# Kernel optimization log

Hardware: AMD Instinct MI355X
Metric: run time of the kernel (lower is better)

Reference implementation:

```python
import jax, jax.numpy as jnp
import numpy as np

SIZE_IN = 4096
SIZE_OUT = 4096
BATCH = 4096


def setup_inputs() -> dict:
    key = jax.random.key(0)
    k1, k2, k3, k4, k5, k6 = jax.random.split(key, 6)
    mu_in = jax.random.normal(k1, (BATCH, SIZE_IN), dtype=jnp.float32)
    sigma_in = jax.random.uniform(k2, (BATCH, SIZE_IN), dtype=jnp.float32)
    # parameters, initialized as in the torch module
    w_mu = 5e-05 * jax.random.normal(k3, (SIZE_IN, SIZE_OUT), dtype=jnp.float32)
    w_sigma = jax.random.uniform(k4, (SIZE_IN * SIZE_OUT,), dtype=jnp.float32,
                                 minval=-12.0, maxval=-2.2)
    b_mu = 5e-05 * jax.random.normal(k5, (SIZE_OUT,), dtype=jnp.float32)
    b_sigma = jax.random.uniform(k6, (SIZE_OUT,), dtype=jnp.float32,
                                 minval=-12.0, maxval=-10.0)
    return {"mu_in": mu_in, "sigma_in": sigma_in, "w_mu": w_mu,
            "w_sigma": w_sigma, "b_mu": b_mu, "b_sigma": b_sigma}


def reference(mu_in, sigma_in, w_mu, w_sigma, b_mu, b_sigma):
    # mean path: mu_out[b,o] = sum_i mu_in[b,i] * w_mu[i,o] + b_mu[o]
    mu_out = jnp.einsum('bi,io->bo', mu_in, w_mu) + b_mu
    # variance path: x diag(softplus(w_sigma)) x^T, per output feature.
    # Equivalent to (mu_in^2) @ softplus(w_sigma).reshape(size_in, size_out),
    # avoiding the quadratic diag_embed + bmm materialization.
    sigma_w = jax.nn.softplus(w_sigma).reshape(SIZE_IN, SIZE_OUT)
    Sigma_out = jnp.einsum('bi,io->bo', mu_in * mu_in, sigma_w) + jax.nn.softplus(b_sigma)
    # KL loss, verbatim from the torch code
    sp = jax.nn.softplus(w_sigma)
    term1 = SIZE_IN * jnp.log(sp)
    term2 = jnp.sum(jnp.abs(w_mu))
    term3 = SIZE_IN * sp
    kl_loss = -0.5 * jnp.mean(term1 - term2 - term3)
    return (mu_out, Sigma_out, kl_loss)
```

## Files before the change

kernel.cpp:

```cpp
#include <hip/hip_runtime.h>
#include <hip/hip_bf16.h>
#include <math.h>

#define M_BATCH   4096
#define K_IN      4096
#define N_OUT     4096
#define NELEM     16777216

typedef __bf16 bf16;
typedef bf16  bf16x8 __attribute__((ext_vector_type(8)));
typedef float f32x4  __attribute__((ext_vector_type(4)));

__device__ __forceinline__ float softplus_fast(float x) {
    if (x > 15.f) return x;
    const float e = __expf(x);
    if (e < 0.0883f)
        return e * (1.f + e * (-0.5f + e * 0.3333333f));
    return __logf(1.f + e);
}

__device__ __forceinline__ unsigned short f2bf_bits(float x) {
    bf16 b = (bf16)x;
    return __builtin_bit_cast(unsigned short, b);
}

__device__ __forceinline__ void gload_lds16(const void* g, void* l) {
    __builtin_amdgcn_global_load_lds(
        (__attribute__((address_space(1))) void*)g,
        (__attribute__((address_space(3))) void*)l,
        16, 0, 0);
}

__global__ __launch_bounds__(256) void prep_a(const float4* __restrict__ mu,
                                              ushort4* __restrict__ A,
                                              ushort4* __restrict__ A2) {
    const int i = blockIdx.x * 256 + threadIdx.x;
    const float4 v = mu[i];
    ushort4 a, a2;
    a.x  = f2bf_bits(v.x);       a.y  = f2bf_bits(v.y);
    a.z  = f2bf_bits(v.z);       a.w  = f2bf_bits(v.w);
    a2.x = f2bf_bits(v.x * v.x); a2.y = f2bf_bits(v.y * v.y);
    a2.z = f2bf_bits(v.z * v.z); a2.w = f2bf_bits(v.w * v.w);
    A[i]  = a;
    A2[i] = a2;
}

__global__ __launch_bounds__(256) void prep_w(const float* __restrict__ wmu,
                                              const float* __restrict__ wsg,
                                              bf16* __restrict__ Wmu_t,
                                              bf16* __restrict__ Wsg_t,
                                              float* __restrict__ partials) {
    __shared__ bf16 tmu[64][65];
    __shared__ bf16 tsg[64][65];
    __shared__ float red[256];

    const int t  = threadIdx.x;
    const int ti = blockIdx.y;
    const int tj = blockIdx.x;
    const int r  = t >> 4;
    const int c4 = (t & 15) << 2;

    float s_abs = 0.f, s_sp = 0.f, s_log = 0.f;

    for (int rr = 0; rr < 64; rr += 16) {
        const int row = rr + r;
        const size_t goff = (size_t)(ti * 64 + row) * N_OUT + tj * 64 + c4;
        const float4 vm = *(const float4*)(wmu + goff);
        const float4 vs = *(const float4*)(wsg + goff);
        const float sp0 = softplus_fast(vs.x), sp1 = softplus_fast(vs.y);
        const float sp2 = softplus_fast(vs.z), sp3 = softplus_fast(vs.w);
        s_abs += fabsf(vm.x) + fabsf(vm.y) + fabsf(vm.z) + fabsf(vm.w);
        s_sp  += sp0 + sp1 + sp2 + sp3;
        s_log += __logf(sp0) + __logf(sp1) + __logf(sp2) + __logf(sp3);
        tmu[row][c4 + 0] = (bf16)vm.x; tmu[row][c4 + 1] = (bf16)vm.y;
        tmu[row][c4 + 2] = (bf16)vm.z; tmu[row][c4 + 3] = (bf16)vm.w;
        tsg[row][c4 + 0] = (bf16)sp0;  tsg[row][c4 + 1] = (bf16)sp1;
        tsg[row][c4 + 2] = (bf16)sp2;  tsg[row][c4 + 3] = (bf16)sp3;
    }
    __syncthreads();

    for (int cc = 0; cc < 64; cc += 16) {
        const int j  = cc + r;
        const int i0 = c4;
        ushort4 om, os;
        om.x = __builtin_bit_cast(unsigned short, tmu[i0 + 0][j]);
        om.y = __builtin_bit_cast(unsigned short, tmu[i0 + 1][j]);
        om.z = __builtin_bit_cast(unsigned short, tmu[i0 + 2][j]);
        om.w = __builtin_bit_cast(unsigned short, tmu[i0 + 3][j]);
        os.x = __builtin_bit_cast(unsigned short, tsg[i0 + 0][j]);
        os.y = __builtin_bit_cast(unsigned short, tsg[i0 + 1][j]);
        os.z = __builtin_bit_cast(unsigned short, tsg[i0 + 2][j]);
        os.w = __builtin_bit_cast(unsigned short, tsg[i0 + 3][j]);
        const size_t o = (size_t)(tj * 64 + j) * K_IN + ti * 64 + i0;
        *(ushort4*)(Wmu_t + o) = om;
        *(ushort4*)(Wsg_t + o) = os;
    }

    const int bid = blockIdx.y * 64 + blockIdx.x;
    float vals[3] = { s_log, s_sp, s_abs };
    for (int v = 0; v < 3; v++) {
        __syncthreads();
        red[t] = vals[v];
        __syncthreads();
        for (int s = 128; s > 0; s >>= 1) {
            if (t < s) red[t] += red[t + s];
            __syncthreads();
        }
        if (t == 0) partials[v * 4096 + bid] = red[0];
    }
}

__global__ __launch_bounds__(256) void gemm_bf16(const bf16* __restrict__ A1,
                                                 const bf16* __restrict__ Bt1,
                                                 const float* __restrict__ bias1,
                                                 float* __restrict__ C1,
                                                 const bf16* __restrict__ A2_,
                                                 const bf16* __restrict__ Bt2,
                                                 const float* __restrict__ bias2,
                                                 float* __restrict__ C2) {
    __shared__ bf16 As[128 * 32];
    __shared__ bf16 Bs[128 * 32];

    const int z = blockIdx.z;
    const bf16*  A    = z ? A2_   : A1;
    const bf16*  Bt   = z ? Bt2   : Bt1;
    const float* bias = z ? bias2 : bias1;
    float*       C    = z ? C2    : C1;

    const int t = threadIdx.x;
    const int rowBase = blockIdx.y * 128;
    const int colBase = blockIdx.x * 128;

    const int srow  = t >> 2;
    const int cg    = ((t & 3) - ((t >> 3) & 3)) & 3;
    const char* agp = (const char*)(A  + (size_t)(rowBase + srow) * K_IN) + (cg << 4);
    const char* bgp = (const char*)(Bt + (size_t)(colBase + srow) * K_IN) + (cg << 4);
    char* alp = (char*)As + t * 16;
    char* blp = (char*)Bs + t * 16;
    const size_t rowskip = (size_t)64 * K_IN * 2;

    const int lane = t & 63;
    const int wave = t >> 6;
    const int wm = (wave >> 1) << 6;
    const int wn = (wave & 1) << 6;
    const int frow = lane & 15;
    const int ko2 = ((((lane >> 4) + (frow >> 1)) & 3) << 3);

    f32x4 zero = { 0.f, 0.f, 0.f, 0.f };
    f32x4 acc[4][4];
#pragma unroll
    for (int i = 0; i < 4; i++)
#pragma unroll
        for (int j = 0; j < 4; j++) acc[i][j] = zero;

    for (int k0 = 0; k0 < K_IN; k0 += 32) {
        const int kb = k0 * 2;
        gload_lds16(agp + kb,            alp);
        gload_lds16(agp + kb + rowskip,  alp + 64 * 64);
        gload_lds16(bgp + kb,            blp);
        gload_lds16(bgp + kb + rowskip,  blp + 64 * 64);
        __syncthreads();

        bf16x8 af[4], bfr[4];
#pragma unroll
        for (int i = 0; i < 4; i++)
            af[i] = *(const bf16x8*)(As + (wm + i * 16 + frow) * 32 + ko2);
#pragma unroll
        for (int j = 0; j < 4; j++)
            bfr[j] = *(const bf16x8*)(Bs + (wn + j * 16 + frow) * 32 + ko2);
#pragma unroll
        for (int i = 0; i < 4; i++)
#pragma unroll
            for (int j = 0; j < 4; j++)
                acc[i][j] = __builtin_amdgcn_mfma_f32_16x16x32_bf16(
                    af[i], bfr[j], acc[i][j], 0, 0, 0);
        __syncthreads();
    }

    const int r0 = (lane >> 4) << 2;
#pragma unroll
    for (int j = 0; j < 4; j++) {
        const int c = colBase + wn + j * 16 + (lane & 15);
        float b = bias[c];
        if (z) b = softplus_fast(b);
#pragma unroll
        for (int i = 0; i < 4; i++) {
            const int rbase = rowBase + wm + i * 16 + r0;
#pragma unroll
            for (int reg = 0; reg < 4; reg++)
                C[(size_t)(rbase + reg) * N_OUT + c] = acc[i][j][reg] + b;
        }
    }
}

__global__ __launch_bounds__(256) void kl_finish(const float* __restrict__ partials,
                                                 const int n,
                                                 float* __restrict__ out) {
    __shared__ double red[256];
    const int t = threadIdx.x;
    double sums[3];
    for (int v = 0; v < 3; v++) {
        double a = 0.0;
        for (int i = t; i < n; i += 256) a += (double)partials[v * n + i];
        red[t] = a;
        __syncthreads();
        for (int s = 128; s > 0; s >>= 1) {
            if (t < s) red[t] += red[t + s];
            __syncthreads();
        }
        sums[v] = red[0];
        __syncthreads();
    }
    if (t == 0) {
        const double mean_log = sums[0] / 16777216.0;
        const double mean_sp  = sums[1] / 16777216.0;
        const double kl = -0.5 * (4096.0 * mean_log - sums[2] - 4096.0 * mean_sp);
        out[0] = (float)kl;
    }
}

__global__ void fb_partials(const float* __restrict__ wmu,
                            const float* __restrict__ wsg,
                            float* __restrict__ partials) {
    __shared__ float red[256];
    const int t = threadIdx.x;
    float s_abs = 0.f, s_sp = 0.f, s_log = 0.f;
    for (int i = blockIdx.x * 256 + t; i < NELEM; i += 1024 * 256) {
        s_abs += fabsf(wmu[i]);
        const float sp = softplus_fast(wsg[i]);
        s_sp += sp;
        s_log += __logf(sp);
    }
    float vals[3] = { s_log, s_sp, s_abs };
    for (int v = 0; v < 3; v++) {
        __syncthreads();
        red[t] = vals[v];
        __syncthreads();
        for (int s = 128; s > 0; s >>= 1) {
            if (t < s) red[t] += red[t + s];
            __syncthreads();
        }
        if (t == 0) partials[v * 1024 + blockIdx.x] = red[0];
    }
}

__global__ void fb_gemm(const float* __restrict__ A,
                        const float* __restrict__ Wm,
                        const float* __restrict__ Ws,
                        const float* __restrict__ bmu,
                        const float* __restrict__ bsg,
                        float* __restrict__ Cmu,
                        float* __restrict__ Csg) {
    __shared__ float As_[16][17], Bm[16][17], Bs_[16][17];
    const int tx = threadIdx.x, ty = threadIdx.y;
    const int row = blockIdx.y * 16 + ty;
    const int col = blockIdx.x * 16 + tx;
    float am = 0.f, as = 0.f;
    for (int k0 = 0; k0 < K_IN; k0 += 16) {
        As_[ty][tx] = A[(size_t)row * K_IN + k0 + tx];
        Bm[ty][tx]  = Wm[(size_t)(k0 + ty) * N_OUT + col];
        Bs_[ty][tx] = softplus_fast(Ws[(size_t)(k0 + ty) * N_OUT + col]);
        __syncthreads();
#pragma unroll
        for (int kk = 0; kk < 16; kk++) {
            const float av = As_[ty][kk];
            am += av * Bm[kk][tx];
            as += av * av * Bs_[kk][tx];
        }
        __syncthreads();
    }
    Cmu[(size_t)row * N_OUT + col] = am + bmu[col];
    Csg[(size_t)row * N_OUT + col] = as + softplus_fast(bsg[col]);
}

extern "C" void kernel_launch(void* const* d_in, const int* in_sizes, int n_in,
                              void* d_out, int out_size, void* d_ws, size_t ws_size,
                              hipStream_t stream) {
    const float* mu_in   = (const float*)d_in[0];
    const float* w_mu    = (const float*)d_in[2];
    const float* w_sigma = (const float*)d_in[3];
    const float* b_mu    = (const float*)d_in[4];
    const float* b_sigma = (const float*)d_in[5];

    float* out_mu  = (float*)d_out;
    float* out_sig = out_mu + (size_t)NELEM;
    float* out_kl  = out_mu + 2 * (size_t)NELEM;

    const size_t mat  = (size_t)NELEM;
    const size_t need = mat * 2 * 4  + 3 * 4096 * sizeof(float);

    if (ws_size >= need) {
        bf16* A      = (bf16*)d_ws;
        bf16* A2     = A + mat;
        bf16* Wmu_t  = A2 + mat;
        bf16* Wsg_t  = Wmu_t + mat;
        float* parts = (float*)(Wsg_t + mat);

        prep_a<<<NELEM / 4 / 256, 256, 0, stream>>>(
            (const float4*)mu_in, (ushort4*)A, (ushort4*)A2);
        prep_w<<<dim3(64, 64), 256, 0, stream>>>(
            w_mu, w_sigma, Wmu_t, Wsg_t, parts);
        gemm_bf16<<<dim3(32, 32, 2), 256, 0, stream>>>(
            A, Wmu_t, b_mu, out_mu, A2, Wsg_t, b_sigma, out_sig);
        kl_finish<<<1, 256, 0, stream>>>(parts, 4096, out_kl);
    } else {
        float* parts = (float*)d_ws;
        fb_partials<<<1024, 256, 0, stream>>>(w_mu, w_sigma, parts);
        fb_gemm<<<dim3(256, 256), dim3(16, 16), 0, stream>>>(
            mu_in, w_mu, w_sigma, b_mu, b_sigma, out_mu, out_sig);
        kl_finish<<<1, 256, 0, stream>>>(parts, 1024, out_kl);
    }
}
```

Measured before the change: 637.5 us.

## Rewrite bf16 GEMM as 256x256 tiles with double-buffered LDS pipeline

The GEMM moves from 128x128 tiles with K=32 steps and 256 threads to 256x256 tiles with K=64 steps and 512 threads (8 waves, each computing 128x64). LDS is double-buffered, and the global-to-LDS loads for the next K tile are interleaved with the MFMA phases. Ordering relies on explicit vmcnt waits, s_barrier, sched_barrier and setprio. The block index is swizzled so neighbouring blocks share L2, and LDS chunks are XOR-swizzled to avoid bank conflicts. Intended gains are more data reuse and hiding memory latency behind compute, at the cost of much higher register and LDS pressure (128 KB of LDS per block) and fragile hand-tuned synchronization.

New measurement: 587.0 us. 7.9% less time.

```diff
diff --git a/kernel.cpp b/kernel.cpp
--- a/kernel.cpp
+++ b/kernel.cpp
@@ -110,16 +110,16 @@
     }
 }
 
-__global__ __launch_bounds__(256) void gemm_bf16(const bf16* __restrict__ A1,
-                                                 const bf16* __restrict__ Bt1,
-                                                 const float* __restrict__ bias1,
-                                                 float* __restrict__ C1,
-                                                 const bf16* __restrict__ A2_,
-                                                 const bf16* __restrict__ Bt2,
-                                                 const float* __restrict__ bias2,
-                                                 float* __restrict__ C2) {
-    __shared__ bf16 As[128 * 32];
-    __shared__ bf16 Bs[128 * 32];
+#define MFMA_BF16 __builtin_amdgcn_mfma_f32_16x16x32_bf16
+
+__global__ __launch_bounds__(512, 2) void gemm_bf16(
+    const bf16* __restrict__ A1,  const bf16* __restrict__ Bt1,
+    const float* __restrict__ bias1, float* __restrict__ C1,
+    const bf16* __restrict__ A2_, const bf16* __restrict__ Bt2,
+    const float* __restrict__ bias2, float* __restrict__ C2) {
+
+    __shared__ bf16 As[2 * 256 * 64];
+    __shared__ bf16 Bs[2 * 256 * 64];
 
     const int z = blockIdx.z;
     const bf16*  A    = z ? A2_   : A1;
@@ -128,69 +128,137 @@
     float*       C    = z ? C2    : C1;
 
     const int t = threadIdx.x;
-    const int rowBase = blockIdx.y * 128;
-    const int colBase = blockIdx.x * 128;
-
-    const int srow  = t >> 2;
-    const int cg    = ((t & 3) - ((t >> 3) & 3)) & 3;
-    const char* agp = (const char*)(A  + (size_t)(rowBase + srow) * K_IN) + (cg << 4);
-    const char* bgp = (const char*)(Bt + (size_t)(colBase + srow) * K_IN) + (cg << 4);
-    char* alp = (char*)As + t * 16;
-    char* blp = (char*)Bs + t * 16;
-    const size_t rowskip = (size_t)64 * K_IN * 2;
+    const int id  = blockIdx.y * 16 + blockIdx.x;
+    const int swz = (id & 7) * 32 + (id >> 3);
+    const int rowBase = (swz >> 4) << 8;
+    const int colBase = (swz & 15) << 8;
+
+    const int srow   = t >> 3;
+    const int schunk = (t & 7) ^ (srow & 7);
+    const char* aG = (const char*)(A  + (size_t)(rowBase + srow) * K_IN + schunk * 8);
+    const char* bG = (const char*)(Bt + (size_t)(colBase + srow) * K_IN + schunk * 8);
+    char* aL = (char*)As + t * 16;
+    char* bL = (char*)Bs + t * 16;
+
+#define STAGE_A(kt, h, par) do {                                               \
+        const size_t kb_ = (size_t)((kt) & 63) << 7;                           \
+        gload_lds16(aG + kb_ + (size_t)(h) * (128 * K_IN * 2),                 \
+                    aL + ((par) << 15) + ((h) << 14));                         \
+        gload_lds16(aG + kb_ + (size_t)(h) * (128 * K_IN * 2) + 64 * K_IN * 2, \
+                    aL + ((par) << 15) + ((h) << 14) + 8192);                  \
+    } while (0)
+#define STAGE_B(kt, h, par) do {                                               \
+        const size_t kb_ = (size_t)((kt) & 63) << 7;                           \
+        gload_lds16(bG + kb_ + (size_t)(h) * (128 * K_IN * 2),                 \
+                    bL + ((par) << 15) + ((h) << 14));                         \
+        gload_lds16(bG + kb_ + (size_t)(h) * (128 * K_IN * 2) + 64 * K_IN * 2, \
+                    bL + ((par) << 15) + ((h) << 14) + 8192);                  \
+    } while (0)
 
     const int lane = t & 63;
     const int wave = t >> 6;
-    const int wm = (wave >> 1) << 6;
-    const int wn = (wave & 1) << 6;
+    const int wr = wave >> 2;
+    const int wc = wave & 3;
     const int frow = lane & 15;
-    const int ko2 = ((((lane >> 4) + (frow >> 1)) & 3) << 3);
-
-    f32x4 zero = { 0.f, 0.f, 0.f, 0.f };
-    f32x4 acc[4][4];
-#pragma unroll
-    for (int i = 0; i < 4; i++)
-#pragma unroll
-        for (int j = 0; j < 4; j++) acc[i][j] = zero;
-
-    for (int k0 = 0; k0 < K_IN; k0 += 32) {
-        const int kb = k0 * 2;
-        gload_lds16(agp + kb,            alp);
-        gload_lds16(agp + kb + rowskip,  alp + 64 * 64);
-        gload_lds16(bgp + kb,            blp);
-        gload_lds16(bgp + kb + rowskip,  blp + 64 * 64);
-        __syncthreads();
-
-        bf16x8 af[4], bfr[4];
-#pragma unroll
-        for (int i = 0; i < 4; i++)
-            af[i] = *(const bf16x8*)(As + (wm + i * 16 + frow) * 32 + ko2);
-#pragma unroll
-        for (int j = 0; j < 4; j++)
-            bfr[j] = *(const bf16x8*)(Bs + (wn + j * 16 + frow) * 32 + ko2);
-#pragma unroll
-        for (int i = 0; i < 4; i++)
-#pragma unroll
-            for (int j = 0; j < 4; j++)
-                acc[i][j] = __builtin_amdgcn_mfma_f32_16x16x32_bf16(
-                    af[i], bfr[j], acc[i][j], 0, 0, 0);
-        __syncthreads();
-    }
+    const int blk0 = (lane >> 4) ^ (lane & 7);
+    const int c0 = blk0 << 4;
+    const int c1 = (blk0 ^ 4) << 4;
+    const char* aRd = (const char*)As + ((wr << 7) + frow) * 128;
+    const char* bRd = (const char*)Bs + ((wc << 6) + frow) * 128;
+
+#define DS_A(par, fi, ck) (*(const bf16x8*)(aRd + ((par) << 15) + ((fi) << 11) + (ck)))
+#define DS_B(par, n,  ck) (*(const bf16x8*)(bRd + ((par) << 15) + ((n)  << 11) + (ck)))
+
+    const f32x4 zero = { 0.f, 0.f, 0.f, 0.f };
+    f32x4 acc[8][4];
+#pragma unroll
+    for (int m = 0; m < 8; ++m)
+#pragma unroll
+        for (int n = 0; n < 4; ++n) acc[m][n] = zero;
+
+#define PHASE(par, q, STAGE_STMT, VM) do {                                        \
+        if ((q) == 0) {                                                           \
+            _Pragma("unroll")                                                     \
+            for (int n = 0; n < 4; ++n) {                                         \
+                bfrag[n][0] = DS_B(par, n, c0);                                   \
+                bfrag[n][1] = DS_B(par, n, c1);                                   \
+            }                                                                     \
+        }                                                                         \
+        const bf16x8 a0k0 = DS_A(par, (q) * 2 + 0, c0);                           \
+        const bf16x8 a0k1 = DS_A(par, (q) * 2 + 0, c1);                           \
+        const bf16x8 a1k0 = DS_A(par, (q) * 2 + 1, c0);                           \
+        const bf16x8 a1k1 = DS_A(par, (q) * 2 + 1, c1);                           \
+        STAGE_STMT;                                                               \
+        if (VM) asm volatile("s_waitcnt vmcnt(4)" ::: "memory");                  \
+        __builtin_amdgcn_sched_barrier(0);                                        \
+        __builtin_amdgcn_s_barrier();                                             \
+        __builtin_amdgcn_sched_barrier(0);                                        \
+        __builtin_amdgcn_s_setprio(1);                                            \
+        _Pragma("unroll")                                                         \
+        for (int n = 0; n < 4; ++n) {                                             \
+            acc[(q)*2+0][n] = MFMA_BF16(a0k0, bfrag[n][0], acc[(q)*2+0][n],0,0,0);\
+            acc[(q)*2+0][n] = MFMA_BF16(a0k1, bfrag[n][1], acc[(q)*2+0][n],0,0,0);\
+            acc[(q)*2+1][n] = MFMA_BF16(a1k0, bfrag[n][0], acc[(q)*2+1][n],0,0,0);\
+            acc[(q)*2+1][n] = MFMA_BF16(a1k1, bfrag[n][1], acc[(q)*2+1][n],0,0,0);\
+        }                                                                         \
+        __builtin_amdgcn_s_setprio(0);                                            \
+        __builtin_amdgcn_sched_barrier(0);                                        \
+        __builtin_amdgcn_s_barrier();                                             \
+        __builtin_amdgcn_sched_barrier(0);                                        \
+    } while (0)
+
+    STAGE_A(0, 0, 0); STAGE_A(0, 1, 0);
+    STAGE_B(0, 0, 0); STAGE_B(0, 1, 0);
+    STAGE_A(1, 0, 1); STAGE_A(1, 1, 1);
+    STAGE_B(1, 0, 1); STAGE_B(1, 1, 1);
+    asm volatile("s_waitcnt vmcnt(8)" ::: "memory");
+    __builtin_amdgcn_sched_barrier(0);
+    __builtin_amdgcn_s_barrier();
+    __builtin_amdgcn_sched_barrier(0);
+
+    for (int i = 0; i < 32; ++i) {
+        const int kA1 = 2 * i + 1;
+        const int kB0 = 2 * i + 2;
+        const int kA0 = 2 * i + 2;
+        const int kB1 = 2 * i + 3;
+        {
+            bf16x8 bfrag[4][2];
+            PHASE(0, 0, STAGE_A(kA1, 0, 1), 0);
+            PHASE(0, 1, STAGE_A(kA1, 1, 1), 0);
+            PHASE(0, 2, STAGE_B(kB0, 0, 0), 0);
+            PHASE(0, 3, STAGE_B(kB0, 1, 0), 1);
+        }
+        {
+            bf16x8 bfrag[4][2];
+            PHASE(1, 0, STAGE_A(kA0, 0, 0), 0);
+            PHASE(1, 1, STAGE_A(kA0, 1, 0), 0);
+            PHASE(1, 2, STAGE_B(kB1, 0, 1), 0);
+            PHASE(1, 3, STAGE_B(kB1, 1, 1), 1);
+        }
+    }
+
+    asm volatile("s_waitcnt vmcnt(0)" ::: "memory");
 
     const int r0 = (lane >> 4) << 2;
-#pragma unroll
-    for (int j = 0; j < 4; j++) {
-        const int c = colBase + wn + j * 16 + (lane & 15);
+    const int ccol = colBase + (wc << 6) + (lane & 15);
+#pragma unroll
+    for (int n = 0; n < 4; ++n) {
+        const int c = ccol + n * 16;
         float b = bias[c];
         if (z) b = softplus_fast(b);
 #pragma unroll
-        for (int i = 0; i < 4; i++) {
-            const int rbase = rowBase + wm + i * 16 + r0;
-#pragma unroll
-            for (int reg = 0; reg < 4; reg++)
-                C[(size_t)(rbase + reg) * N_OUT + c] = acc[i][j][reg] + b;
-        }
-    }
+        for (int m = 0; m < 8; ++m) {
+            const int rbase = rowBase + (wr << 7) + (m << 4) + r0;
+#pragma unroll
+            for (int reg = 0; reg < 4; ++reg)
+                C[(size_t)(rbase + reg) * N_OUT + c] = acc[m][n][reg] + b;
+        }
+    }
+#undef STAGE_A
+#undef STAGE_B
+#undef DS_A
+#undef DS_B
+#undef PHASE
 }
 
 __global__ __launch_bounds__(256) void kl_finish(const float* __restrict__ partials,
@@ -300,7 +368,7 @@
             (const float4*)mu_in, (ushort4*)A, (ushort4*)A2);
         prep_w<<<dim3(64, 64), 256, 0, stream>>>(
             w_mu, w_sigma, Wmu_t, Wsg_t, parts);
-        gemm_bf16<<<dim3(32, 32, 2), 256, 0, stream>>>(
+        gemm_bf16<<<dim3(16, 16, 2), 512, 0, stream>>>(
             A, Wmu_t, b_mu, out_mu, A2, Wsg_t, b_sigma, out_sig);
         kl_finish<<<1, 256, 0, stream>>>(parts, 4096, out_kl);
     } else {
```
